# Kernel optimization log

Measured on AMD Instinct MI355X. Metric: run time of the kernel, lower is better.

The kernel has to match this reference:

```python
import jax, jax.numpy as jnp
import numpy as np

K = 20
EPS = 1e-5
NEG_SLOPE = 0.2


def _knn_idx(x, k):
    # x: (B, N, C). Torch: pd = -||xi||^2 + 2 xi.xj - ||xj||^2, topk largest = nearest.
    inner = jnp.einsum('bnc,bmc->bnm', x, x)
    xx = jnp.sum(x * x, axis=-1)  # (B, N)
    pd = 2.0 * inner - xx[:, :, None] - xx[:, None, :]
    _, idx = jax.lax.top_k(pd, k)  # (B, N, k)
    return idx


def _bn_lrelu(h, gamma, beta, axes):
    mean = jnp.mean(h, axis=axes)
    var = jnp.var(h, axis=axes)  # biased, as in torch BN training normalization
    hn = (h - mean) * jax.lax.rsqrt(var + EPS) * gamma + beta
    return jnp.where(hn >= 0, hn, NEG_SLOPE * hn)


def _edge_conv(x, W, gamma, beta, k):
    # x: (B, N, C); W: (O, 2C). Returns (B, N, O).
    idx = _knn_idx(x, k)
    nbr = jax.vmap(lambda xb, ib: xb[ib])(x, idx)  # (B, N, k, C) gather
    center = jnp.broadcast_to(x[:, :, None, :], nbr.shape)
    edge = jnp.concatenate([nbr - center, center], axis=-1)  # (B, N, k, 2C)
    h = jnp.einsum('bnkc,oc->bnko', edge, W)
    h = _bn_lrelu(h, gamma, beta, axes=(0, 1, 2))
    return jnp.max(h, axis=2)  # max over k -> (B, N, O)


def setup_inputs() -> dict:
    key = jax.random.key(0)
    ks = jax.random.split(key, 16)
    B, N = 32, 1024
    d = {'x': jax.random.normal(ks[0], (B, N, 3), dtype=jnp.float32)}
    dims = [(64, 6), (64, 128), (128, 128), (256, 256), (1024, 512)]
    for i, (o, c) in enumerate(dims, start=1):
        d[f'W{i}'] = jax.random.normal(ks[i], (o, c), dtype=jnp.float32) * 0.05
        d[f'g{i}'] = jnp.ones((o,), dtype=jnp.float32)
        d[f'b{i}'] = jnp.zeros((o,), dtype=jnp.float32)
    return d


def reference(x, W1, g1, b1, W2, g2, b2, W3, g3, b3, W4, g4, b4, W5, g5, b5):
    B = x.shape[0]
    x1 = _edge_conv(x, W1, g1, b1, K)    # (B, N, 64)
    x2 = _edge_conv(x1, W2, g2, b2, K)   # (B, N, 64)
    x3 = _edge_conv(x2, W3, g3, b3, K)   # (B, N, 128)
    x4 = _edge_conv(x3, W4, g4, b4, K)   # (B, N, 256)
    cat = jnp.concatenate([x1, x2, x3, x4], axis=-1)  # (B, N, 512)
    h = jnp.einsum('bnc,oc->bno', cat, W5)            # (B, N, 1024)
    h = _bn_lrelu(h, g5, b5, axes=(0, 1))
    out = jnp.max(h, axis=1)  # adaptive max pool over points -> (B, 1024)
    return out.reshape(B, 1, -1)
```

## Files before the change

### kernel.cpp

```cpp
#include <hip/hip_runtime.h>
#include <math.h>

#define BB 32
#define NN 1024
#define KNNK 20
#define PTS (BB*NN)

typedef __attribute__((ext_vector_type(8)))  short short8;
typedef __attribute__((ext_vector_type(4)))  float f32x4;
typedef __attribute__((ext_vector_type(16))) float f32x16;

__device__ __forceinline__ float lrelu(float v){ return v >= 0.f ? v : 0.2f*v; }

__device__ __forceinline__ unsigned short f2b(float x){
    union { float f; unsigned u; } c; c.f = x;
    unsigned r = c.u + 0x7FFFu + ((c.u >> 16) & 1u);
    return (unsigned short)(r >> 16);
}

__global__ void sq_kernel(const float* __restrict__ x, int stride, int C, float* __restrict__ xx){
    int pn = blockIdx.x*256 + threadIdx.x;
    if (pn >= PTS) return;
    const float* r = x + (size_t)pn*stride;
    float s = 0.f;
    for (int c = 0; c < C; ++c){ float v = r[c]; s = fmaf(v, v, s); }
    xx[pn] = s;
}

template<int C>
__global__ void __launch_bounds__(256) dist_kernel(const float* __restrict__ x, int stride,
                                                   const float* __restrict__ xx,
                                                   float* __restrict__ D, int b0){
    constexpr int KC = (C < 32 ? C : 32);
    __shared__ float As[KC][132];
    __shared__ float Bs[KC][132];
    const int tid = threadIdx.x;
    int t = blockIdx.x, ti = 0;
    while (t >= 8 - ti){ t -= 8 - ti; ++ti; }
    const int tj = ti + t;
    const int i0 = ti*128, j0 = tj*128;
    const int bl = blockIdx.z;
    const int b  = b0 + bl;
    const float* xb = x + (size_t)b*NN*stride;
    const int rt = tid >> 4, ct = tid & 15;
    float acc[8][8] = {{0.f}};

    for (int kc = 0; kc < C; kc += KC){
        __syncthreads();
        if constexpr (KC % 4 == 0){
            for (int i = tid; i < 128*(KC/4); i += 256){
                int kq = i % (KC/4), rr = i / (KC/4);
                float4 va = *(const float4*)&xb[(size_t)(i0+rr)*stride + kc + kq*4];
                As[kq*4+0][rr]=va.x; As[kq*4+1][rr]=va.y; As[kq*4+2][rr]=va.z; As[kq*4+3][rr]=va.w;
                float4 vb = *(const float4*)&xb[(size_t)(j0+rr)*stride + kc + kq*4];
                Bs[kq*4+0][rr]=vb.x; Bs[kq*4+1][rr]=vb.y; Bs[kq*4+2][rr]=vb.z; Bs[kq*4+3][rr]=vb.w;
            }
        } else {
            for (int i = tid; i < 128*KC; i += 256){
                int k = i % KC, rr = i / KC;
                As[k][rr] = xb[(size_t)(i0+rr)*stride + kc + k];
                Bs[k][rr] = xb[(size_t)(j0+rr)*stride + kc + k];
            }
        }
        __syncthreads();
        #pragma unroll
        for (int k = 0; k < KC; ++k){
            float4 a0 = *(const float4*)&As[k][rt*8];
            float4 a1 = *(const float4*)&As[k][rt*8+4];
            float4 b0v= *(const float4*)&Bs[k][ct*8];
            float4 b1v= *(const float4*)&Bs[k][ct*8+4];
            float av[8]={a0.x,a0.y,a0.z,a0.w,a1.x,a1.y,a1.z,a1.w};
            float bw[8]={b0v.x,b0v.y,b0v.z,b0v.w,b1v.x,b1v.y,b1v.z,b1v.w};
            #pragma unroll
            for (int i = 0; i < 8; ++i)
                #pragma unroll
                for (int j = 0; j < 8; ++j)
                    acc[i][j] = fmaf(av[i], bw[j], acc[i][j]);
        }
    }
    const float* xxb = xx + b*NN;
    float xi[8], xj[8];
    #pragma unroll
    for (int i=0;i<8;++i) xi[i] = xxb[i0 + rt*8 + i];
    #pragma unroll
    for (int j=0;j<8;++j) xj[j] = xxb[j0 + ct*8 + j];
    #pragma unroll
    for (int i=0;i<8;++i){
        float4 d0, d1;
        d0.x = 2.f*acc[i][0] - xi[i] - xj[0];
        d0.y = 2.f*acc[i][1] - xi[i] - xj[1];
        d0.z = 2.f*acc[i][2] - xi[i] - xj[2];
        d0.w = 2.f*acc[i][3] - xi[i] - xj[3];
        d1.x = 2.f*acc[i][4] - xi[i] - xj[4];
        d1.y = 2.f*acc[i][5] - xi[i] - xj[5];
        d1.z = 2.f*acc[i][6] - xi[i] - xj[6];
        d1.w = 2.f*acc[i][7] - xi[i] - xj[7];
        float* drow = &D[((size_t)bl*NN + i0 + rt*8 + i)*NN + j0 + ct*8];
        *(float4*)drow = d0;
        *(float4*)(drow+4) = d1;
    }
    if (ti != tj){
        #pragma unroll
        for (int j=0;j<8;++j){
            float4 m0, m1;
            m0.x = 2.f*acc[0][j] - xj[j] - xi[0];
            m0.y = 2.f*acc[1][j] - xj[j] - xi[1];
            m0.z = 2.f*acc[2][j] - xj[j] - xi[2];
            m0.w = 2.f*acc[3][j] - xj[j] - xi[3];
            m1.x = 2.f*acc[4][j] - xj[j] - xi[4];
            m1.y = 2.f*acc[5][j] - xj[j] - xi[5];
            m1.z = 2.f*acc[6][j] - xj[j] - xi[6];
            m1.w = 2.f*acc[7][j] - xj[j] - xi[7];
            float* mrow = &D[((size_t)bl*NN + j0 + ct*8 + j)*NN + i0 + rt*8];
            *(float4*)mrow = m0;
            *(float4*)(mrow+4) = m1;
        }
    }
}

__global__ void __launch_bounds__(256) topk_kernel(const float* __restrict__ D,
                                                   int* __restrict__ idxout, int baseRow){
    const int tid = threadIdx.x;
    const int wv = tid >> 6, lane = tid & 63;
    const int rid = blockIdx.x*4 + wv;
    const float* drow = D + (size_t)rid * NN;
    unsigned u[16];
    #pragma unroll
    for (int i = 0; i < 16; ++i){
        unsigned bits = __float_as_uint(drow[i*64 + lane]);
        unsigned m = (bits & 0x80000000u) ? 0xFFFFFFFFu : 0x80000000u;
        u[i] = bits ^ m;
    }
    unsigned t = 0u;
    for (int b = 31; b >= 0; --b){
        unsigned cand = t | (1u << b);
        int cnt = 0;
        #pragma unroll
        for (int i = 0; i < 16; ++i)
            cnt += (int)__popcll(__ballot(u[i] >= cand));
        if (cnt >= KNNK) t = cand;
    }
    const unsigned long long lt = (lane == 0) ? 0ull : ((~0ull) >> (64 - lane));
    int* orow = idxout + ((size_t)baseRow + rid) * KNNK;
    int cbase = 0;
    #pragma unroll
    for (int i = 0; i < 16; ++i){
        bool gt2 = (u[i] > t);
        unsigned long long mask = __ballot(gt2);
        if (gt2) orow[cbase + (int)__popcll(mask & lt)] = i*64 + lane;
        cbase += (int)__popcll(mask);
    }
    for (int i = 0; i < 16; ++i){
        if (cbase >= KNNK) break;
        bool eq = (u[i] == t);
        unsigned long long mask = __ballot(eq);
        int pos = cbase + (int)__popcll(mask & lt);
        if (eq && pos < KNNK) orow[pos] = i*64 + lane;
        cbase += (int)__popcll(mask);
    }
}

template<int C, int O>
__global__ void __launch_bounds__(256) gemmG_kernel(const float* __restrict__ x, int stride,
                                                    const float* __restrict__ W,
                                                    float* __restrict__ G1, float* __restrict__ Gd){
    constexpr int KC = (C < 32 ? C : 32);
    __shared__ float Xl [KC][68];
    __shared__ float W1l[KC][68];
    __shared__ float W2l[KC][68];
    const int tid = threadIdx.x;
    const int r0 = blockIdx.x * 64;
    const int o0 = blockIdx.y * 64;
    const int rt = tid & 15, ct = tid >> 4;

    float a1[4][4] = {{0.f}}, a2[4][4] = {{0.f}};
    for (int kc = 0; kc < C; kc += KC){
        __syncthreads();
        for (int i = tid; i < KC*64; i += 256){
            int k = i % KC, rr = i / KC;
            Xl [k][rr] = x[(size_t)(r0+rr)*stride + kc + k];
            W1l[k][rr] = W[(size_t)(o0+rr)*(2*C) + kc + k];
            W2l[k][rr] = W[(size_t)(o0+rr)*(2*C) + C + kc + k];
        }
        __syncthreads();
        #pragma unroll
        for (int k = 0; k < KC; ++k){
            float4 xa = *(const float4*)&Xl [k][rt*4];
            float4 w1 = *(const float4*)&W1l[k][ct*4];
            float4 w2 = *(const float4*)&W2l[k][ct*4];
            float xv[4] = {xa.x, xa.y, xa.z, xa.w};
            #pragma unroll
            for (int i = 0; i < 4; ++i){
                a1[i][0] = fmaf(xv[i], w1.x, a1[i][0]);
                a1[i][1] = fmaf(xv[i], w1.y, a1[i][1]);
                a1[i][2] = fmaf(xv[i], w1.z, a1[i][2]);
                a1[i][3] = fmaf(xv[i], w1.w, a1[i][3]);
                a2[i][0] = fmaf(xv[i], w2.x, a2[i][0]);
                a2[i][1] = fmaf(xv[i], w2.y, a2[i][1]);
                a2[i][2] = fmaf(xv[i], w2.z, a2[i][2]);
                a2[i][3] = fmaf(xv[i], w2.w, a2[i][3]);
            }
        }
    }
    #pragma unroll
    for (int i = 0; i < 4; ++i){
        size_t row = (size_t)(r0 + rt*4 + i);
        float4 g1v = make_float4(a1[i][0], a1[i][1], a1[i][2], a1[i][3]);
        float4 gdv = make_float4(a2[i][0]-a1[i][0], a2[i][1]-a1[i][1],
                                 a2[i][2]-a1[i][2], a2[i][3]-a1[i][3]);
        *(float4*)&G1[row*O + o0 + ct*4] = g1v;
        *(float4*)&Gd[row*O + o0 + ct*4] = gdv;
    }
}

template<int O>
__global__ void __launch_bounds__(256) gather_kernel(const float* __restrict__ G1,
                                                     const float* __restrict__ Gd,
                                                     const int* __restrict__ idxg, int bgbase,
                                                     float* __restrict__ catslice,
                                                     float* __restrict__ stats){
    constexpr int OG = O/4;
    constexpr int PP = 256/OG;
    constexpr int NP = 16;
    __shared__ int nbs[NP][KNNK];
    const int tid = threadIdx.x;
    const int p0 = blockIdx.x * NP;
    for (int i = tid; i < NP*KNNK; i += 256){
        int pp = i / KNNK, kk = i - pp*KNNK;
        int pl = p0 + pp;
        nbs[pp][kk] = ((pl >> 10) << 10) + idxg[(size_t)(bgbase + pl)*KNNK + kk];
    }
    __syncthreads();
    const int o4 = (tid % OG)*4;
    const int pq = tid / OG;
    float S1[4] = {0.f,0.f,0.f,0.f}, S2[4] = {0.f,0.f,0.f,0.f};
    for (int pp = pq; pp < NP; pp += PP){
        int pl = p0 + pp;
        float4 dv = *(const float4*)&Gd[(size_t)pl*O + o4];
        float d[4] = {dv.x, dv.y, dv.z, dv.w};
        float mx[4] = {-INFINITY,-INFINITY,-INFINITY,-INFINITY};
        float ls[4] = {0.f,0.f,0.f,0.f}, lq[4] = {0.f,0.f,0.f,0.f};
        #pragma unroll
        for (int kk = 0; kk < KNNK; ++kk){
            float4 gv = *(const float4*)&G1[(size_t)nbs[pp][kk]*O + o4];
            float ga[4] = {gv.x, gv.y, gv.z, gv.w};
            #pragma unroll
            for (int c = 0; c < 4; ++c){
                mx[c] = fmaxf(mx[c], ga[c]);
                ls[c] += ga[c];
                lq[c] = fmaf(ga[c], ga[c], lq[c]);
            }
        }
        float4 outv;
        float* op = &outv.x;
        #pragma unroll
        for (int c = 0; c < 4; ++c){
            S1[c] += ls[c] + 20.f*d[c];
            S2[c] += lq[c] + 2.f*d[c]*ls[c] + 20.f*d[c]*d[c];
            op[c] = mx[c] + d[c];
        }
        *(float4*)&catslice[(size_t)(bgbase + pl)*512 + o4] = outv;
    }
    int rep = blockIdx.x & 63;
    #pragma unroll
    for (int c = 0; c < 4; ++c){
        atomicAdd(&stats[rep*2*O + o4 + c],     S1[c]);
        atomicAdd(&stats[rep*2*O + O + o4 + c], S2[c]);
    }
}

__global__ void fin_kernel(const float* __restrict__ stats, int O, float cnt,
                           float* __restrict__ mean, float* __restrict__ invstd){
    int o = threadIdx.x;
    if (o >= O) return;
    float s1 = 0.f, s2 = 0.f;
    for (int r = 0; r < 64; ++r){
        s1 += stats[r*2*O + o];
        s2 += stats[r*2*O + O + o];
    }
    float m = s1 / cnt;
    float v = s2 / cnt - m*m;
    mean[o] = m;
    invstd[o] = rsqrtf(v + 1e-5f);
}

template<int O>
__global__ void apply_kernel(float* __restrict__ catslice,
                             const float* __restrict__ mean, const float* __restrict__ invstd,
                             const float* __restrict__ g, const float* __restrict__ bt){
    int i = blockIdx.x*256 + threadIdx.x;
    int pn = i / O, o = i - pn*O;
    float* p = &catslice[(size_t)pn*512 + o];
    float hn = (*p - mean[o]) * invstd[o] * g[o] + bt[o];
    *p = lrelu(hn);
}

__global__ void tob16_kernel(const float* __restrict__ src, unsigned short* __restrict__ dst, int n4){
    int i = blockIdx.x*256 + threadIdx.x;
    if (i >= n4) return;
    float4 v = *(const float4*)&src[(size_t)i*4];
    ushort4 o;
    o.x = f2b(v.x); o.y = f2b(v.y); o.z = f2b(v.z); o.w = f2b(v.w);
    *(ushort4*)&dst[(size_t)i*4] = o;
}

__global__ void __launch_bounds__(256) l5m_kernel(const unsigned short* __restrict__ Am,
                                                  const unsigned short* __restrict__ Bm,
                                                  float* __restrict__ pmax,
                                                  float* __restrict__ psum,
                                                  float* __restrict__ psq){
    __shared__ __align__(16) unsigned short As[128][64];
    __shared__ __align__(16) unsigned short Bs[128][64];
    const int tid = threadIdx.x;
    const int r0 = blockIdx.x * 128;
    const int o0 = blockIdx.y * 128;
    const int w = tid >> 6, lane = tid & 63;
    const int m32 = lane & 31, kh = lane >> 5;
    const int wm = (w & 1) * 64;
    const int wn = (w >> 1) * 64;

    f32x16 acc[2][2];
    #pragma unroll
    for (int i=0;i<2;++i)
        #pragma unroll
        for (int j=0;j<2;++j)
            #pragma unroll
            for (int r=0;r<16;++r) acc[i][j][r] = 0.f;

    for (int kc = 0; kc < 512; kc += 64){
        __syncthreads();
        #pragma unroll
        for (int t = 0; t < 4; ++t){
            int i = tid + t*256;
            int rr = i >> 3, ch = i & 7;
            int sl = ch ^ (rr & 7);
            *(uint4*)&As[rr][sl*8] = *(const uint4*)&Am[(size_t)(r0+rr)*512 + kc + ch*8];
            *(uint4*)&Bs[rr][sl*8] = *(const uint4*)&Bm[(size_t)(o0+rr)*512 + kc + ch*8];
        }
        __syncthreads();
        #pragma unroll
        for (int q = 0; q < 4; ++q){
            int lk = q*2 + kh;
            short8 a[2], bfr[2];
            #pragma unroll
            for (int mb = 0; mb < 2; ++mb){
                int rA = wm + mb*32 + m32;
                a[mb] = *(const short8*)&As[rA][(lk ^ (rA & 7))*8];
            }
            #pragma unroll
            for (int nb = 0; nb < 2; ++nb){
                int rB = wn + nb*32 + m32;
                bfr[nb] = *(const short8*)&Bs[rB][(lk ^ (rB & 7))*8];
            }
            #pragma unroll
            for (int mb = 0; mb < 2; ++mb)
                #pragma unroll
                for (int nb = 0; nb < 2; ++nb)
                    acc[mb][nb] = __builtin_amdgcn_mfma_f32_32x32x16_bf16(a[mb], bfr[nb], acc[mb][nb], 0, 0, 0);
        }
    }
    __syncthreads();
    float* red = (float*)&As[0][0];
    #pragma unroll
    for (int nb = 0; nb < 2; ++nb){
        float mx = -INFINITY, s1 = 0.f, s2 = 0.f;
        #pragma unroll
        for (int mb = 0; mb < 2; ++mb)
            #pragma unroll
            for (int r = 0; r < 16; ++r){
                float v = acc[mb][nb][r];
                mx = fmaxf(mx, v); s1 += v; s2 = fmaf(v, v, s2);
            }
        mx = fmaxf(mx, __shfl_xor(mx, 32));
        s1 += __shfl_xor(s1, 32);
        s2 += __shfl_xor(s2, 32);
        if (lane < 32){
            int col = wn + nb*32 + m32;
            float* p = red + ((size_t)(w & 1) * 128 + col) * 3;
            p[0] = mx; p[1] = s1; p[2] = s2;
        }
    }
    __syncthreads();
    if (tid < 128){
        const float* p0 = red + (size_t)tid*3;
        const float* p1 = red + (size_t)(128 + tid)*3;
        float mx = fmaxf(p0[0], p1[0]);
        float s1 = p0[1] + p1[1];
        float s2 = p0[2] + p1[2];
        size_t pi = (size_t)blockIdx.x*1024 + o0 + tid;
        pmax[pi] = mx; psum[pi] = s1; psq[pi] = s2;
    }
}

__global__ void fin5_kernel(const float* __restrict__ pmax, const float* __restrict__ psum,
                            const float* __restrict__ psq,
                            const float* __restrict__ g, const float* __restrict__ bt,
                            float* __restrict__ out){
    int o = blockIdx.x*256 + threadIdx.x;
    float s1 = 0.f, s2 = 0.f;
    for (int r = 0; r < 256; ++r){
        s1 += psum[(size_t)r*1024 + o];
        s2 += psq [(size_t)r*1024 + o];
    }
    float m  = s1 / 32768.f;
    float v  = s2 / 32768.f - m*m;
    float is = rsqrtf(v + 1e-5f);
    float gg = g[o], bb2 = bt[o];
    for (int b = 0; b < 32; ++b){
        float mx = -INFINITY;
        #pragma unroll
        for (int ns = 0; ns < 8; ++ns) mx = fmaxf(mx, pmax[((size_t)b*8 + ns)*1024 + o]);
        float hn = (mx - m) * is * gg + bb2;
        out[(size_t)b*1024 + o] = lrelu(hn);
    }
}

extern "C" void kernel_launch(void* const* d_in, const int* in_sizes, int n_in,
                              void* d_out, int out_size, void* d_ws, size_t ws_size,
                              hipStream_t stream) {
    (void)in_sizes; (void)n_in; (void)out_size;
    const float* x  = (const float*)d_in[0];
    const float* W1 = (const float*)d_in[1];  const float* g1 = (const float*)d_in[2];  const float* b1 = (const float*)d_in[3];
    const float* W2 = (const float*)d_in[4];  const float* g2 = (const float*)d_in[5];  const float* b2 = (const float*)d_in[6];
    const float* W3 = (const float*)d_in[7];  const float* g3 = (const float*)d_in[8];  const float* b3 = (const float*)d_in[9];
    const float* W4 = (const float*)d_in[10]; const float* g4 = (const float*)d_in[11]; const float* b4 = (const float*)d_in[12];
    const float* W5 = (const float*)d_in[13]; const float* g5 = (const float*)d_in[14]; const float* b5 = (const float*)d_in[15];
    float* out = (float*)d_out;

    const size_t fixedBytes = (size_t)PTS*512*4 + (size_t)PTS*KNNK*4 + (size_t)PTS*4
                            + (size_t)64*2*256*4 + 2048*4 + 3*(size_t)256*1024*4
                            + (size_t)1024*512*2;
    int CB;
    if      (ws_size >= fixedBytes + (size_t)32*NN*NN*4) CB = 32;
    else if (ws_size >= fixedBytes + (size_t)16*NN*NN*4) CB = 16;
    else                                                 CB = 8;
    const size_t Rbytes = (size_t)CB*NN*NN*4;

    char* wsp = (char*)d_ws;
    float* cat    = (float*)wsp; wsp += (size_t)PTS*512*4;
    char*  R      = wsp;         wsp += Rbytes;
    int*   idx    = (int*)  wsp; wsp += (size_t)PTS*KNNK*4;
    float* xx     = (float*)wsp; wsp += (size_t)PTS*4;
    float* stats  = (float*)wsp; wsp += (size_t)64*2*256*4;
    float* mean   = (float*)wsp; wsp += 1024*4;
    float* invstd = (float*)wsp; wsp += 1024*4;
    float* pmax   = (float*)wsp; wsp += (size_t)256*1024*4;
    float* psum   = (float*)wsp; wsp += (size_t)256*1024*4;
    float* psq    = (float*)wsp; wsp += (size_t)256*1024*4;
    unsigned short* W5b = (unsigned short*)wsp; wsp += (size_t)1024*512*2;

    float* Dbuf  = (float*)R;
    float* G1    = (float*)R;
    float* GdS   = (float*)(R + (size_t)16*1024*1024);
    float* GdB   = (float*)(R + (size_t)32*1024*1024);
    unsigned short* catB = (unsigned short*)R;

    const float cntE = (float)(PTS*KNNK);
    const int nch = 32 / CB;
    const bool bigG = (Rbytes >= (size_t)64*1024*1024);

    sq_kernel<<<PTS/256, 256, 0, stream>>>(x, 3, 3, xx);
    for (int bc = 0; bc < nch; ++bc){
        dist_kernel<3><<<dim3(36,1,CB), 256, 0, stream>>>(x, 3, xx, Dbuf, bc*CB);
        topk_kernel<<<CB*1024/4, 256, 0, stream>>>(Dbuf, idx, bc*CB*1024);
    }
    hipMemsetAsync(stats, 0, 64*2*256*4, stream);
    gemmG_kernel<3,64><<<dim3(512,1), 256, 0, stream>>>(x, 3, W1, G1, GdS);
    gather_kernel<64><<<2048, 256, 0, stream>>>(G1, GdS, idx, 0, cat + 0, stats);
    fin_kernel<<<1, 64, 0, stream>>>(stats, 64, cntE, mean, invstd);
    apply_kernel<64><<<PTS*64/256, 256, 0, stream>>>(cat + 0, mean, invstd, g1, b1);

    sq_kernel<<<PTS/256, 256, 0, stream>>>(cat + 0, 512, 64, xx);
    for (int bc = 0; bc < nch; ++bc){
        dist_kernel<64><<<dim3(36,1,CB), 256, 0, stream>>>(cat + 0, 512, xx, Dbuf, bc*CB);
        topk_kernel<<<CB*1024/4, 256, 0, stream>>>(Dbuf, idx, bc*CB*1024);
    }
    hipMemsetAsync(stats, 0, 64*2*256*4, stream);
    gemmG_kernel<64,64><<<dim3(512,1), 256, 0, stream>>>(cat + 0, 512, W2, G1, GdS);
    gather_kernel<64><<<2048, 256, 0, stream>>>(G1, GdS, idx, 0, cat + 64, stats);
    fin_kernel<<<1, 64, 0, stream>>>(stats, 64, cntE, mean, invstd);
    apply_kernel<64><<<PTS*64/256, 256, 0, stream>>>(cat + 64, mean, invstd, g2, b2);

    sq_kernel<<<PTS/256, 256, 0, stream>>>(cat + 64, 512, 64, xx);
    for (int bc = 0; bc < nch; ++bc){
        dist_kernel<64><<<dim3(36,1,CB), 256, 0, stream>>>(cat + 64, 512, xx, Dbuf, bc*CB);
        topk_kernel<<<CB*1024/4, 256, 0, stream>>>(Dbuf, idx, bc*CB*1024);
    }
    hipMemsetAsync(stats, 0, 64*2*256*4, stream);
    gemmG_kernel<64,128><<<dim3(512,2), 256, 0, stream>>>(cat + 64, 512, W3, G1, GdS);
    gather_kernel<128><<<2048, 256, 0, stream>>>(G1, GdS, idx, 0, cat + 128, stats);
    fin_kernel<<<1, 128, 0, stream>>>(stats, 128, cntE, mean, invstd);
    apply_kernel<128><<<PTS*128/256, 256, 0, stream>>>(cat + 128, mean, invstd, g3, b3);

    sq_kernel<<<PTS/256, 256, 0, stream>>>(cat + 128, 512, 128, xx);
    for (int bc = 0; bc < nch; ++bc){
        dist_kernel<128><<<dim3(36,1,CB), 256, 0, stream>>>(cat + 128, 512, xx, Dbuf, bc*CB);
        topk_kernel<<<CB*1024/4, 256, 0, stream>>>(Dbuf, idx, bc*CB*1024);
    }
    hipMemsetAsync(stats, 0, 64*2*256*4, stream);
    if (bigG){
        gemmG_kernel<128,256><<<dim3(512,4), 256, 0, stream>>>(cat + 128, 512, W4, G1, GdB);
        gather_kernel<256><<<2048, 256, 0, stream>>>(G1, GdB, idx, 0, cat + 256, stats);
    } else {
        for (int bg = 0; bg < 4; ++bg){
            gemmG_kernel<128,256><<<dim3(128,4), 256, 0, stream>>>(cat + 128 + (size_t)bg*8192*512, 512, W4, G1, GdS);
            gather_kernel<256><<<512, 256, 0, stream>>>(G1, GdS, idx, bg*8192, cat + 256, stats);
        }
    }
    fin_kernel<<<1, 256, 0, stream>>>(stats, 256, cntE, mean, invstd);
    apply_kernel<256><<<PTS*256/256, 256, 0, stream>>>(cat + 256, mean, invstd, g4, b4);

    tob16_kernel<<<PTS*512/4/256, 256, 0, stream>>>(cat, catB, PTS*512/4);
    tob16_kernel<<<1024*512/4/256, 256, 0, stream>>>(W5, W5b, 1024*512/4);
    l5m_kernel<<<dim3(256, 8), 256, 0, stream>>>(catB, W5b, pmax, psum, psq);
    fin5_kernel<<<4, 256, 0, stream>>>(pmax, psum, psq, g5, b5, out);
}
```

Before: 1.235 ms.

## Fuse pairwise distance computation with top-k selection into one kNN kernel

Replaces the separate distance GEMM, which wrote a full N×N matrix per batch to global memory, and the top-k kernel that read it back. The new kernel computes distances for 16 rows per block while streaming all 1024 candidate points through shared memory, keeps the 4×1024 row values in registers per wave, and runs the radix-select top-k directly on them. It removes the large D-buffer write and read plus the batch-chunk launch loop. In exchange it gives up the symmetric tile reuse and the 8×8 register blocking of the old GEMM, which reloads the B points for every 16-row block and uses more registers (64 floats of distances per thread).

```diff
diff --git a/kernel.cpp b/kernel.cpp
--- a/kernel.cpp
+++ b/kernel.cpp
@@ -28,135 +28,135 @@
 }
 
 template<int C>
-__global__ void __launch_bounds__(256) dist_kernel(const float* __restrict__ x, int stride,
+__global__ void __launch_bounds__(256) knnf_kernel(const float* __restrict__ x, int stride,
                                                    const float* __restrict__ xx,
-                                                   float* __restrict__ D, int b0){
-    constexpr int KC = (C < 32 ? C : 32);
-    __shared__ float As[KC][132];
-    __shared__ float Bs[KC][132];
+                                                   int* __restrict__ idxout){
+    constexpr int KCH = (C >= 16) ? 16 : C;
+    __shared__ float As[16][C+4];
+    __shared__ float Bs[256][KCH+4];
     const int tid = threadIdx.x;
-    int t = blockIdx.x, ti = 0;
-    while (t >= 8 - ti){ t -= 8 - ti; ++ti; }
-    const int tj = ti + t;
-    const int i0 = ti*128, j0 = tj*128;
-    const int bl = blockIdx.z;
-    const int b  = b0 + bl;
-    const float* xb = x + (size_t)b*NN*stride;
-    const int rt = tid >> 4, ct = tid & 15;
-    float acc[8][8] = {{0.f}};
-
-    for (int kc = 0; kc < C; kc += KC){
-        __syncthreads();
-        if constexpr (KC % 4 == 0){
-            for (int i = tid; i < 128*(KC/4); i += 256){
-                int kq = i % (KC/4), rr = i / (KC/4);
-                float4 va = *(const float4*)&xb[(size_t)(i0+rr)*stride + kc + kq*4];
-                As[kq*4+0][rr]=va.x; As[kq*4+1][rr]=va.y; As[kq*4+2][rr]=va.z; As[kq*4+3][rr]=va.w;
-                float4 vb = *(const float4*)&xb[(size_t)(j0+rr)*stride + kc + kq*4];
-                Bs[kq*4+0][rr]=vb.x; Bs[kq*4+1][rr]=vb.y; Bs[kq*4+2][rr]=vb.z; Bs[kq*4+3][rr]=vb.w;
-            }
-        } else {
-            for (int i = tid; i < 128*KC; i += 256){
-                int k = i % KC, rr = i / KC;
-                As[k][rr] = xb[(size_t)(i0+rr)*stride + kc + k];
-                Bs[k][rr] = xb[(size_t)(j0+rr)*stride + kc + k];
-            }
-        }
-        __syncthreads();
-        #pragma unroll
-        for (int k = 0; k < KC; ++k){
-            float4 a0 = *(const float4*)&As[k][rt*8];
-            float4 a1 = *(const float4*)&As[k][rt*8+4];
-            float4 b0v= *(const float4*)&Bs[k][ct*8];
-            float4 b1v= *(const float4*)&Bs[k][ct*8+4];
-            float av[8]={a0.x,a0.y,a0.z,a0.w,a1.x,a1.y,a1.z,a1.w};
-            float bw[8]={b0v.x,b0v.y,b0v.z,b0v.w,b1v.x,b1v.y,b1v.z,b1v.w};
-            #pragma unroll
-            for (int i = 0; i < 8; ++i)
+    const int w = tid >> 6, lane = tid & 63;
+    const int bt = blockIdx.y;
+    const int row0 = blockIdx.x * 16;
+    const int wrow = w*4;
+    const float* xb = x + (size_t)bt*NN*stride;
+
+    if constexpr (C % 4 == 0){
+        for (int i = tid; i < 16*(C/4); i += 256){
+            int rr = i/(C/4), c4 = i%(C/4);
+            *(float4*)&As[rr][c4*4] = *(const float4*)&xb[(size_t)(row0+rr)*stride + c4*4];
+        }
+    } else {
+        for (int i = tid; i < 16*C; i += 256){
+            int rr = i/C, c = i%C;
+            As[rr][c] = xb[(size_t)(row0+rr)*stride + c];
+        }
+    }
+    float xi[4];
+    #pragma unroll
+    for (int r=0;r<4;++r) xi[r] = xx[bt*NN + row0 + wrow + r];
+
+    float v[4][16];
+    for (int jp = 0; jp < 4; ++jp){
+        #pragma unroll
+        for (int r=0;r<4;++r)
+            #pragma unroll
+            for (int c=0;c<4;++c) v[r][jp*4+c] = 0.f;
+        for (int kc = 0; kc < C; kc += KCH){
+            __syncthreads();
+            {
+                const float* src = &xb[(size_t)(jp*256 + tid)*stride + kc];
+                if constexpr (KCH % 4 == 0){
+                    #pragma unroll
+                    for (int k4 = 0; k4 < KCH/4; ++k4)
+                        *(float4*)&Bs[tid][k4*4] = *(const float4*)&src[k4*4];
+                } else {
+                    #pragma unroll
+                    for (int k = 0; k < KCH; ++k) Bs[tid][k] = src[k];
+                }
+            }
+            __syncthreads();
+            if constexpr (KCH % 4 == 0){
                 #pragma unroll
-                for (int j = 0; j < 8; ++j)
-                    acc[i][j] = fmaf(av[i], bw[j], acc[i][j]);
-        }
-    }
-    const float* xxb = xx + b*NN;
-    float xi[8], xj[8];
-    #pragma unroll
-    for (int i=0;i<8;++i) xi[i] = xxb[i0 + rt*8 + i];
-    #pragma unroll
-    for (int j=0;j<8;++j) xj[j] = xxb[j0 + ct*8 + j];
-    #pragma unroll
-    for (int i=0;i<8;++i){
-        float4 d0, d1;
-        d0.x = 2.f*acc[i][0] - xi[i] - xj[0];
-        d0.y = 2.f*acc[i][1] - xi[i] - xj[1];
-        d0.z = 2.f*acc[i][2] - xi[i] - xj[2];
-        d0.w = 2.f*acc[i][3] - xi[i] - xj[3];
-        d1.x = 2.f*acc[i][4] - xi[i] - xj[4];
-        d1.y = 2.f*acc[i][5] - xi[i] - xj[5];
-        d1.z = 2.f*acc[i][6] - xi[i] - xj[6];
-        d1.w = 2.f*acc[i][7] - xi[i] - xj[7];
-        float* drow = &D[((size_t)bl*NN + i0 + rt*8 + i)*NN + j0 + ct*8];
-        *(float4*)drow = d0;
-        *(float4*)(drow+4) = d1;
-    }
-    if (ti != tj){
-        #pragma unroll
-        for (int j=0;j<8;++j){
-            float4 m0, m1;
-            m0.x = 2.f*acc[0][j] - xj[j] - xi[0];
-            m0.y = 2.f*acc[1][j] - xj[j] - xi[1];
-            m0.z = 2.f*acc[2][j] - xj[j] - xi[2];
-            m0.w = 2.f*acc[3][j] - xj[j] - xi[3];
-            m1.x = 2.f*acc[4][j] - xj[j] - xi[4];
-            m1.y = 2.f*acc[5][j] - xj[j] - xi[5];
-            m1.z = 2.f*acc[6][j] - xj[j] - xi[6];
-            m1.w = 2.f*acc[7][j] - xj[j] - xi[7];
-            float* mrow = &D[((size_t)bl*NN + j0 + ct*8 + j)*NN + i0 + rt*8];
-            *(float4*)mrow = m0;
-            *(float4*)(mrow+4) = m1;
-        }
-    }
-}
-
-__global__ void __launch_bounds__(256) topk_kernel(const float* __restrict__ D,
-                                                   int* __restrict__ idxout, int baseRow){
-    const int tid = threadIdx.x;
-    const int wv = tid >> 6, lane = tid & 63;
-    const int rid = blockIdx.x*4 + wv;
-    const float* drow = D + (size_t)rid * NN;
-    unsigned u[16];
-    #pragma unroll
-    for (int i = 0; i < 16; ++i){
-        unsigned bits = __float_as_uint(drow[i*64 + lane]);
-        unsigned m = (bits & 0x80000000u) ? 0xFFFFFFFFu : 0x80000000u;
-        u[i] = bits ^ m;
-    }
-    unsigned t = 0u;
-    for (int b = 31; b >= 0; --b){
-        unsigned cand = t | (1u << b);
-        int cnt = 0;
-        #pragma unroll
-        for (int i = 0; i < 16; ++i)
-            cnt += (int)__popcll(__ballot(u[i] >= cand));
-        if (cnt >= KNNK) t = cand;
-    }
+                for (int k4 = 0; k4 < KCH/4; ++k4){
+                    float4 a[4], bb[4];
+                    #pragma unroll
+                    for (int r=0;r<4;++r) a[r] = *(const float4*)&As[wrow+r][kc + k4*4];
+                    #pragma unroll
+                    for (int c=0;c<4;++c) bb[c] = *(const float4*)&Bs[c*64 + lane][k4*4];
+                    #pragma unroll
+                    for (int r=0;r<4;++r)
+                        #pragma unroll
+                        for (int c=0;c<4;++c){
+                            float acc = v[r][jp*4+c];
+                            acc = fmaf(a[r].x, bb[c].x, acc);
+                            acc = fmaf(a[r].y, bb[c].y, acc);
+                            acc = fmaf(a[r].z, bb[c].z, acc);
+                            acc = fmaf(a[r].w, bb[c].w, acc);
+                            v[r][jp*4+c] = acc;
+                        }
+                }
+            } else {
+                #pragma unroll
+                for (int k = 0; k < KCH; ++k){
+                    float a[4], bb[4];
+                    #pragma unroll
+                    for (int r=0;r<4;++r) a[r] = As[wrow+r][kc + k];
+                    #pragma unroll
+                    for (int c=0;c<4;++c) bb[c] = Bs[c*64 + lane][k];
+                    #pragma unroll
+                    for (int r=0;r<4;++r)
+                        #pragma unroll
+                        for (int c=0;c<4;++c)
+                            v[r][jp*4+c] = fmaf(a[r], bb[c], v[r][jp*4+c]);
+                }
+            }
+        }
+        float xj[4];
+        #pragma unroll
+        for (int c=0;c<4;++c) xj[c] = xx[bt*NN + jp*256 + c*64 + lane];
+        #pragma unroll
+        for (int r=0;r<4;++r)
+            #pragma unroll
+            for (int c=0;c<4;++c)
+                v[r][jp*4+c] = 2.f*v[r][jp*4+c] - xi[r] - xj[c];
+    }
+
     const unsigned long long lt = (lane == 0) ? 0ull : ((~0ull) >> (64 - lane));
-    int* orow = idxout + ((size_t)baseRow + rid) * KNNK;
-    int cbase = 0;
-    #pragma unroll
-    for (int i = 0; i < 16; ++i){
-        bool gt2 = (u[i] > t);
-        unsigned long long mask = __ballot(gt2);
-        if (gt2) orow[cbase + (int)__popcll(mask & lt)] = i*64 + lane;
-        cbase += (int)__popcll(mask);
-    }
-    for (int i = 0; i < 16; ++i){
-        if (cbase >= KNNK) break;
-        bool eq = (u[i] == t);
-        unsigned long long mask = __ballot(eq);
-        int pos = cbase + (int)__popcll(mask & lt);
-        if (eq && pos < KNNK) orow[pos] = i*64 + lane;
-        cbase += (int)__popcll(mask);
+    #pragma unroll 1
+    for (int r = 0; r < 4; ++r){
+        unsigned u[16];
+        #pragma unroll
+        for (int i = 0; i < 16; ++i){
+            unsigned bits = __float_as_uint(v[r][i]);
+            u[i] = bits ^ ((bits & 0x80000000u) ? 0xFFFFFFFFu : 0x80000000u);
+        }
+        unsigned t = 0u;
+        for (int bit = 31; bit >= 0; --bit){
+            unsigned cand = t | (1u << bit);
+            int cnt = 0;
+            #pragma unroll
+            for (int i = 0; i < 16; ++i)
+                cnt += (int)__popcll(__ballot(u[i] >= cand));
+            if (cnt >= KNNK) t = cand;
+        }
+        int* orow = idxout + ((size_t)bt*NN + row0 + wrow + r) * KNNK;
+        int cbase = 0;
+        #pragma unroll
+        for (int i = 0; i < 16; ++i){
+            bool g = (u[i] > t);
+            unsigned long long mask = __ballot(g);
+            if (g) orow[cbase + (int)__popcll(mask & lt)] = i*64 + lane;
+            cbase += (int)__popcll(mask);
+        }
+        for (int i = 0; i < 16; ++i){
+            if (cbase >= KNNK) break;
+            bool e = (u[i] == t);
+            unsigned long long mask = __ballot(e);
+            int pos = cbase + (int)__popcll(mask & lt);
+            if (e && pos < KNNK) orow[pos] = i*64 + lane;
+            cbase += (int)__popcll(mask);
+        }
     }
 }
 
@@ -430,11 +430,8 @@
     const size_t fixedBytes = (size_t)PTS*512*4 + (size_t)PTS*KNNK*4 + (size_t)PTS*4
                             + (size_t)64*2*256*4 + 2048*4 + 3*(size_t)256*1024*4
                             + (size_t)1024*512*2;
-    int CB;
-    if      (ws_size >= fixedBytes + (size_t)32*NN*NN*4) CB = 32;
-    else if (ws_size >= fixedBytes + (size_t)16*NN*NN*4) CB = 16;
-    else                                                 CB = 8;
-    const size_t Rbytes = (size_t)CB*NN*NN*4;
+    const bool bigG = (ws_size >= fixedBytes + (size_t)64*1024*1024);
+    const size_t Rbytes = bigG ? (size_t)64*1024*1024 : (size_t)32*1024*1024;
 
     char* wsp = (char*)d_ws;
     float* cat    = (float*)wsp; wsp += (size_t)PTS*512*4;
@@ -449,21 +446,15 @@
     float* psq    = (float*)wsp; wsp += (size_t)256*1024*4;
     unsigned short* W5b = (unsigned short*)wsp; wsp += (size_t)1024*512*2;
 
-    float* Dbuf  = (float*)R;
-    float* G1    = (float*)R;
-    float* GdS   = (float*)(R + (size_t)16*1024*1024);
-    float* GdB   = (float*)(R + (size_t)32*1024*1024);
+    float* G1   = (float*)R;
+    float* GdS  = (float*)(R + (size_t)16*1024*1024);
+    float* GdB  = (float*)(R + (size_t)32*1024*1024);
     unsigned short* catB = (unsigned short*)R;
 
     const float cntE = (float)(PTS*KNNK);
-    const int nch = 32 / CB;
-    const bool bigG = (Rbytes >= (size_t)64*1024*1024);
 
     sq_kernel<<<PTS/256, 256, 0, stream>>>(x, 3, 3, xx);
-    for (int bc = 0; bc < nch; ++bc){
-        dist_kernel<3><<<dim3(36,1,CB), 256, 0, stream>>>(x, 3, xx, Dbuf, bc*CB);
-        topk_kernel<<<CB*1024/4, 256, 0, stream>>>(Dbuf, idx, bc*CB*1024);
-    }
+    knnf_kernel<3><<<dim3(64,32), 256, 0, stream>>>(x, 3, xx, idx);
     hipMemsetAsync(stats, 0, 64*2*256*4, stream);
     gemmG_kernel<3,64><<<dim3(512,1), 256, 0, stream>>>(x, 3, W1, G1, GdS);
     gather_kernel<64><<<2048, 256, 0, stream>>>(G1, GdS, idx, 0, cat + 0, stats);
@@ -471,10 +462,7 @@
     apply_kernel<64><<<PTS*64/256, 256, 0, stream>>>(cat + 0, mean, invstd, g1, b1);
 
     sq_kernel<<<PTS/256, 256, 0, stream>>>(cat + 0, 512, 64, xx);
-    for (int bc = 0; bc < nch; ++bc){
-        dist_kernel<64><<<dim3(36,1,CB), 256, 0, stream>>>(cat + 0, 512, xx, Dbuf, bc*CB);
-        topk_kernel<<<CB*1024/4, 256, 0, stream>>>(Dbuf, idx, bc*CB*1024);
-    }
+    knnf_kernel<64><<<dim3(64,32), 256, 0, stream>>>(cat + 0, 512, xx, idx);
     hipMemsetAsync(stats, 0, 64*2*256*4, stream);
     gemmG_kernel<64,64><<<dim3(512,1), 256, 0, stream>>>(cat + 0, 512, W2, G1, GdS);
     gather_kernel<64><<<2048, 256, 0, stream>>>(G1, GdS, idx, 0, cat + 64, stats);
@@ -482,10 +470,7 @@
     apply_kernel<64><<<PTS*64/256, 256, 0, stream>>>(cat + 64, mean, invstd, g2, b2);
 
     sq_kernel<<<PTS/256, 256, 0, stream>>>(cat + 64, 512, 64, xx);
-    for (int bc = 0; bc < nch; ++bc){
-        dist_kernel<64><<<dim3(36,1,CB), 256, 0, stream>>>(cat + 64, 512, xx, Dbuf, bc*CB);
-        topk_kernel<<<CB*1024/4, 256, 0, stream>>>(Dbuf, idx, bc*CB*1024);
-    }
+    knnf_kernel<64><<<dim3(64,32), 256, 0, stream>>>(cat + 64, 512, xx, idx);
     hipMemsetAsync(stats, 0, 64*2*256*4, stream);
     gemmG_kernel<64,128><<<dim3(512,2), 256, 0, stream>>>(cat + 64, 512, W3, G1, GdS);
     gather_kernel<128><<<2048, 256, 0, stream>>>(G1, GdS, idx, 0, cat + 128, stats);
@@ -493,10 +478,7 @@
     apply_kernel<128><<<PTS*128/256, 256, 0, stream>>>(cat + 128, mean, invstd, g3, b3);
 
     sq_kernel<<<PTS/256, 256, 0, stream>>>(cat + 128, 512, 128, xx);
-    for (int bc = 0; bc < nch; ++bc){
-        dist_kernel<128><<<dim3(36,1,CB), 256, 0, stream>>>(cat + 128, 512, xx, Dbuf, bc*CB);
-        topk_kernel<<<CB*1024/4, 256, 0, stream>>>(Dbuf, idx, bc*CB*1024);
-    }
+    knnf_kernel<128><<<dim3(64,32), 256, 0, stream>>>(cat + 128, 512, xx, idx);
     hipMemsetAsync(stats, 0, 64*2*256*4, stream);
     if (bigG){
         gemmG_kernel<128,256><<<dim3(512,4), 256, 0, stream>>>(cat + 128, 512, W4, G1, GdB);
```

Measured after the change: 2.171 ms. +75.8%, slower.
